# Kernel optimization log

Hardware: AMD Instinct MI355X
Metric: run time of the kernel (lower is better)

## Reference

```python
import jax, jax.numpy as jnp
import numpy as np

D_MODEL = 1024
N_HEADS = 16
D_HEAD = D_MODEL // N_HEADS
D_FF = 4096
B, T = 4, 2048
LN_EPS = 1e-5


def _layer_norm(x, gamma, beta):
    mu = jnp.mean(x, axis=-1, keepdims=True)
    var = jnp.var(x, axis=-1, keepdims=True)
    return (x - mu) * jax.lax.rsqrt(var + LN_EPS) * gamma + beta


def setup_inputs() -> dict:
    key = jax.random.key(0)
    ks = jax.random.split(key, 8)
    x = jax.random.normal(ks[0], (B, T, D_MODEL), dtype=jnp.float32)
    # causal mask: True = blocked (upper triangle above diagonal)
    attn_mask = ~jnp.tril(jnp.ones((T, T), dtype=bool))
    # xavier-uniform linear weights stored as [in, out] (pytorch applies x @ W.T)
    def xavier(k, fan_in, fan_out):
        lim = float(np.sqrt(6.0 / (fan_in + fan_out)))
        return jax.random.uniform(k, (fan_in, fan_out), jnp.float32, -lim, lim)
    Wq = xavier(ks[1], D_MODEL, D_MODEL); bq = jnp.zeros((D_MODEL,), jnp.float32)
    Wk = xavier(ks[2], D_MODEL, D_MODEL); bk = jnp.zeros((D_MODEL,), jnp.float32)
    Wv = xavier(ks[3], D_MODEL, D_MODEL); bv = jnp.zeros((D_MODEL,), jnp.float32)
    Wo = xavier(ks[4], D_MODEL, D_MODEL); bo = jnp.zeros((D_MODEL,), jnp.float32)
    W1 = xavier(ks[5], D_MODEL, D_FF); b1 = jnp.zeros((D_FF,), jnp.float32)
    W2 = 0.02 * jax.random.normal(ks[6], (D_FF, D_MODEL), jnp.float32)  # normal std=0.02 per _init_weights
    b2 = jnp.zeros((D_MODEL,), jnp.float32)
    g1 = jnp.ones((D_MODEL,), jnp.float32); be1 = jnp.zeros((D_MODEL,), jnp.float32)
    g2 = jnp.ones((D_MODEL,), jnp.float32); be2 = jnp.zeros((D_MODEL,), jnp.float32)
    return {"x": x, "attn_mask": attn_mask,
            "Wq": Wq, "bq": bq, "Wk": Wk, "bk": bk, "Wv": Wv, "bv": bv,
            "Wo": Wo, "bo": bo, "W1": W1, "b1": b1, "W2": W2, "b2": b2,
            "g1": g1, "be1": be1, "g2": g2, "be2": be2}


def reference(x, attn_mask, Wq, bq, Wk, bk, Wv, bv, Wo, bo, W1, b1, W2, b2, g1, be1, g2, be2):
    Bd, Td, Dd = x.shape
    residual = x
    x_n = _layer_norm(x, g1, be1)
    # projections -> (B, H, T, Dh)
    q = (x_n @ Wq + bq).reshape(Bd, Td, N_HEADS, D_HEAD).transpose(0, 2, 1, 3)
    k = (x_n @ Wk + bk).reshape(Bd, Td, N_HEADS, D_HEAD).transpose(0, 2, 1, 3)
    v = (x_n @ Wv + bv).reshape(Bd, Td, N_HEADS, D_HEAD).transpose(0, 2, 1, 3)
    scale = 1.0 / jnp.sqrt(jnp.asarray(D_HEAD, x.dtype))
    scores = jnp.einsum('bhqd,bhkd->bhqk', q, k) * scale  # (B,H,T,T)
    scores = jnp.where(attn_mask[None, None], -jnp.inf, scores)
    attn = jax.nn.softmax(scores, axis=-1)
    attn_out = jnp.einsum('bhqk,bhkd->bhqd', attn, v)
    attn_out = attn_out.transpose(0, 2, 1, 3).reshape(Bd, Td, Dd)
    attn_out = attn_out @ Wo + bo
    x = residual + attn_out  # dropout = identity (p=0 / eval)
    h = _layer_norm(x, g2, be2)
    h = jax.nn.gelu(h @ W1 + b1, approximate=False) @ W2 + b2
    return x + h
```

## Files before the change

kernel.cpp:

```cpp
#include <hip/hip_runtime.h>
#include <hip/hip_bf16.h>
#include <math.h>

#define TT   2048
#define DD   1024
#define HHD  16
#define FFD  4096
#define NTOK 8192

typedef __attribute__((ext_vector_type(8))) short bf16x8;
typedef __attribute__((ext_vector_type(4))) float f32x4;
typedef unsigned int u32;
#define AS(n) __attribute__((address_space(n)))

__device__ __forceinline__ unsigned short f2bf(float f) {
    u32 u = __builtin_bit_cast(u32, f);
    u += 0x7fffu + ((u >> 16) & 1u);
    return (unsigned short)(u >> 16);
}

__device__ __forceinline__ void gld_lds16(const void* g, void* l) {
    __builtin_amdgcn_global_load_lds((const AS(1) u32*)g, (AS(3) u32*)l, 16, 0, 0);
}

__device__ __forceinline__ int swz(int row) { return (row + (row >> 3)) & 7; }

__global__ __launch_bounds__(256) void wtrans(const float* __restrict__ W,
                                              unsigned short* __restrict__ Wt,
                                              int K, int N) {
    __shared__ float t[32][33];
    int tx = threadIdx.x & 31, ty = threadIdx.x >> 5;
    int n0 = blockIdx.x * 32, k0 = blockIdx.y * 32;
    #pragma unroll
    for (int i = 0; i < 32; i += 8)
        t[ty + i][tx] = W[(size_t)(k0 + ty + i) * N + n0 + tx];
    __syncthreads();
    #pragma unroll
    for (int i = 0; i < 32; i += 8)
        Wt[(size_t)(n0 + ty + i) * K + k0 + tx] = f2bf(t[tx][ty + i]);
}

__global__ __launch_bounds__(256) void ln_bf16(const float* __restrict__ x,
                                               const float* __restrict__ g,
                                               const float* __restrict__ be,
                                               unsigned short* __restrict__ y) {
    int tok = blockIdx.x, tid = threadIdx.x;
    float4 v = ((const float4*)(x + (size_t)tok * DD))[tid];
    float s  = v.x + v.y + v.z + v.w;
    float ss = v.x*v.x + v.y*v.y + v.z*v.z + v.w*v.w;
    #pragma unroll
    for (int m = 32; m >= 1; m >>= 1) { s += __shfl_xor(s, m); ss += __shfl_xor(ss, m); }
    __shared__ float red[8];
    if ((tid & 63) == 0) { red[tid >> 6] = s; red[4 + (tid >> 6)] = ss; }
    __syncthreads();
    s  = red[0] + red[1] + red[2] + red[3];
    ss = red[4] + red[5] + red[6] + red[7];
    float mu   = s * (1.0f / DD);
    float rstd = rsqrtf(ss * (1.0f / DD) - mu * mu + 1e-5f);
    float4 gv = ((const float4*)g)[tid];
    float4 bv = ((const float4*)be)[tid];
    ushort4 o;
    o.x = f2bf((v.x - mu) * rstd * gv.x + bv.x);
    o.y = f2bf((v.y - mu) * rstd * gv.y + bv.y);
    o.z = f2bf((v.z - mu) * rstd * gv.z + bv.z);
    o.w = f2bf((v.w - mu) * rstd * gv.w + bv.w);
    *(ushort4*)(y + (size_t)tok * DD + tid * 4) = o;
}

template <int MODE>
__global__ __launch_bounds__(256, 3) void gemm_bf16(const unsigned short* __restrict__ A,
                                                    const unsigned short* __restrict__ Bt,
                                                    const float* __restrict__ bias,
                                                    void* __restrict__ C,
                                                    const float* __restrict__ resid,
                                                    int M, int N, int K) {
    __shared__ __align__(16) unsigned short As[128 * 64];
    __shared__ __align__(16) unsigned short Bs[128 * 64];
    int tid = threadIdx.x, lane = tid & 63, w = tid >> 6;
    int wm = w >> 1, wn = w & 1;
    int m0 = blockIdx.y * 128, n0 = blockIdx.x * 128;
    int c = lane & 15, g = lane >> 4;

    f32x4 acc[4][4];
    f32x4 z4 = {0.f, 0.f, 0.f, 0.f};
    #pragma unroll
    for (int i = 0; i < 4; ++i)
        #pragma unroll
        for (int j = 0; j < 4; ++j) acc[i][j] = z4;

    const unsigned short* aSrc[4];
    const unsigned short* bSrc[4];
    int ldsOff[4];
    #pragma unroll
    for (int i = 0; i < 4; ++i) {
        int inst = w * 4 + i;
        int row  = inst * 8 + (lane >> 3);
        int kk   = ((lane & 7) ^ swz(row)) << 3;
        aSrc[i] = A  + (size_t)(m0 + row) * K + kk;
        bSrc[i] = Bt + (size_t)(n0 + row) * K + kk;
        ldsOff[i] = inst * 1024;
    }

    for (int k0 = 0; k0 < K; k0 += 64) {
        #pragma unroll
        for (int i = 0; i < 4; ++i) {
            gld_lds16(aSrc[i] + k0, (char*)As + ldsOff[i]);
            gld_lds16(bSrc[i] + k0, (char*)Bs + ldsOff[i]);
        }
        __syncthreads();
        #pragma unroll
        for (int ks = 0; ks < 2; ++ks) {
            bf16x8 af[4], bfr[4];
            int slot = ks * 4 + g;
            #pragma unroll
            for (int f = 0; f < 4; ++f) {
                int ra = wm * 64 + f * 16 + c;
                af[f]  = *(const bf16x8*)((const char*)As + ra * 128 + ((slot ^ swz(ra)) << 4));
                int rb = wn * 64 + f * 16 + c;
                bfr[f] = *(const bf16x8*)((const char*)Bs + rb * 128 + ((slot ^ swz(rb)) << 4));
            }
            #pragma unroll
            for (int i = 0; i < 4; ++i)
                #pragma unroll
                for (int j = 0; j < 4; ++j)
                    acc[i][j] = __builtin_amdgcn_mfma_f32_16x16x32_bf16(af[i], bfr[j], acc[i][j], 0, 0, 0);
        }
        __syncthreads();
    }

    float bcol[4];
    #pragma unroll
    for (int j = 0; j < 4; ++j) bcol[j] = bias[n0 + wn * 64 + j * 16 + c];
    #pragma unroll
    for (int i = 0; i < 4; ++i) {
        #pragma unroll
        for (int r = 0; r < 4; ++r) {
            int rowm = m0 + wm * 64 + i * 16 + g * 4 + r;
            #pragma unroll
            for (int j = 0; j < 4; ++j) {
                float val = acc[i][j][r] + bcol[j];
                int col = n0 + wn * 64 + j * 16 + c;
                if (MODE == 1) {
                    int b = rowm >> 11, t = rowm & 2047, h = col >> 6, d = col & 63;
                    ((unsigned short*)C)[(((size_t)((b << 4) + h) * TT + t) << 6) + d] = f2bf(val);
                } else if (MODE == 2) {
                    size_t idx = (size_t)rowm * N + col;
                    ((float*)C)[idx] = val + resid[idx];
                } else {
                    float ge = 0.5f * val * (1.0f + erff(val * 0.70710678118f));
                    ((unsigned short*)C)[(size_t)rowm * N + col] = f2bf(ge);
                }
            }
        }
    }
}

__global__ __launch_bounds__(256) void attn_bf16(const unsigned short* __restrict__ q,
                                                 const unsigned short* __restrict__ k,
                                                 const unsigned short* __restrict__ v,
                                                 unsigned short* __restrict__ ao) {
    __shared__ __align__(16) unsigned short Ks[64 * 64];
    __shared__ __align__(16) unsigned short Vt[64 * 64];
    __shared__ __align__(16) unsigned short Ps[4][16 * 64];
    int tid = threadIdx.x, lane = tid & 63, w = tid >> 6;
    int qt = blockIdx.x, bh = blockIdx.y;
    int q0 = qt * 64;
    size_t base = (size_t)bh * TT * 64;
    int c = lane & 15, g = lane >> 4;

    int qrow = q0 + w * 16 + c;
    bf16x8 qf[2];
    qf[0] = *(const bf16x8*)(q + base + (size_t)qrow * 64 + g * 8);
    qf[1] = *(const bf16x8*)(q + base + (size_t)qrow * 64 + 32 + g * 8);

    float m_i[4], l_i[4];
    f32x4 o[4];
    f32x4 z4 = {0.f, 0.f, 0.f, 0.f};
    #pragma unroll
    for (int j = 0; j < 4; ++j) { m_i[j] = -INFINITY; l_i[j] = 0.0f; o[j] = z4; }

    const unsigned short* kSrc[2];
    int kOff[2];
    #pragma unroll
    for (int i = 0; i < 2; ++i) {
        int inst = w * 2 + i;
        int row  = inst * 8 + (lane >> 3);
        kSrc[i] = k + base + (size_t)row * 64 + (((lane & 7) ^ swz(row)) << 3);
        kOff[i] = inst * 1024;
    }

    for (int kt = 0; kt <= qt; ++kt) {
        int kv0 = kt * 64;
        __syncthreads();
        #pragma unroll
        for (int i = 0; i < 2; ++i)
            gld_lds16(kSrc[i] + (size_t)kv0 * 64, (char*)Ks + kOff[i]);
        #pragma unroll
        for (int p = 0; p < 2; ++p) {
            int kvr = w * 16 + p * 8 + (lane >> 3);
            int d0  = (lane & 7) * 8;
            bf16x8 vv = *(const bf16x8*)(v + base + (size_t)(kv0 + kvr) * 64 + d0);
            #pragma unroll
            for (int e = 0; e < 8; ++e) {
                int dr = d0 + e;
                int byte = dr * 128 + ((((kvr >> 3) ^ swz(dr)) << 4)) + ((kvr & 7) << 1);
                *(unsigned short*)((char*)Vt + byte) = (unsigned short)vv[e];
            }
        }
        __syncthreads();

        f32x4 s[4];
        #pragma unroll
        for (int f = 0; f < 4; ++f) s[f] = z4;
        #pragma unroll
        for (int ks = 0; ks < 2; ++ks) {
            int slot = ks * 4 + g;
            #pragma unroll
            for (int f = 0; f < 4; ++f) {
                int rb = f * 16 + c;
                bf16x8 kf = *(const bf16x8*)((const char*)Ks + rb * 128 + ((slot ^ swz(rb)) << 4));
                s[f] = __builtin_amdgcn_mfma_f32_16x16x32_bf16(qf[ks], kf, s[f], 0, 0, 0);
            }
        }

        bool diag = (kt == qt);
        #pragma unroll
        for (int j = 0; j < 4; ++j) {
            int lq = g * 4 + j;
            int gq = q0 + w * 16 + lq;
            #pragma unroll
            for (int f = 0; f < 4; ++f) {
                float sv = s[f][j] * 0.125f;
                if (diag && (kv0 + f * 16 + c > gq)) sv = -INFINITY;
                s[f][j] = sv;
            }
            float mx = fmaxf(fmaxf(s[0][j], s[1][j]), fmaxf(s[2][j], s[3][j]));
            #pragma unroll
            for (int mm = 8; mm >= 1; mm >>= 1) mx = fmaxf(mx, __shfl_xor(mx, mm));
            float newm = fmaxf(m_i[j], mx);
            float al = __expf(m_i[j] - newm);
            float rs = 0.0f;
            #pragma unroll
            for (int f = 0; f < 4; ++f) {
                float p = __expf(s[f][j] - newm);
                s[f][j] = p;
                rs += p;
            }
            #pragma unroll
            for (int mm = 8; mm >= 1; mm >>= 1) rs += __shfl_xor(rs, mm);
            l_i[j] = l_i[j] * al + rs;
            m_i[j] = newm;
            #pragma unroll
            for (int f = 0; f < 4; ++f) {
                int col = f * 16 + c;
                int byte = lq * 128 + (((col >> 3) ^ swz(lq)) << 4) + ((col & 7) << 1);
                *(unsigned short*)((char*)Ps[w] + byte) = f2bf(s[f][j]);
            }
            #pragma unroll
            for (int fd = 0; fd < 4; ++fd) o[fd][j] *= al;
        }
        asm volatile("s_waitcnt lgkmcnt(0)" ::: "memory");
        __builtin_amdgcn_sched_barrier(0);

        #pragma unroll
        for (int ks = 0; ks < 2; ++ks) {
            int slot = ks * 4 + g;
            bf16x8 pa = *(const bf16x8*)((const char*)Ps[w] + c * 128 + ((slot ^ swz(c)) << 4));
            #pragma unroll
            for (int fd = 0; fd < 4; ++fd) {
                int rv = fd * 16 + c;
                bf16x8 vf = *(const bf16x8*)((const char*)Vt + rv * 128 + ((slot ^ swz(rv)) << 4));
                o[fd] = __builtin_amdgcn_mfma_f32_16x16x32_bf16(pa, vf, o[fd], 0, 0, 0);
            }
        }
    }

    int b = bh >> 4, h = bh & 15;
    #pragma unroll
    for (int fd = 0; fd < 4; ++fd)
        #pragma unroll
        for (int j = 0; j < 4; ++j) {
            int t = q0 + w * 16 + g * 4 + j;
            float val = o[fd][j] / l_i[j];
            ao[(((size_t)(b * TT + t)) << 10) + (h << 6) + fd * 16 + c] = f2bf(val);
        }
}

extern "C" void kernel_launch(void* const* d_in, const int* in_sizes, int n_in,
                              void* d_out, int out_size, void* d_ws, size_t ws_size,
                              hipStream_t stream) {
    const float* x   = (const float*)d_in[0];
    const float* Wq  = (const float*)d_in[2];
    const float* bq  = (const float*)d_in[3];
    const float* Wk  = (const float*)d_in[4];
    const float* bk  = (const float*)d_in[5];
    const float* Wv  = (const float*)d_in[6];
    const float* bv  = (const float*)d_in[7];
    const float* Wo  = (const float*)d_in[8];
    const float* bo  = (const float*)d_in[9];
    const float* W1  = (const float*)d_in[10];
    const float* b1  = (const float*)d_in[11];
    const float* W2  = (const float*)d_in[12];
    const float* b2  = (const float*)d_in[13];
    const float* g1  = (const float*)d_in[14];
    const float* be1 = (const float*)d_in[15];
    const float* g2  = (const float*)d_in[16];
    const float* be2 = (const float*)d_in[17];

    float* out = (float*)d_out;
    char* w = (char*)d_ws;
    const size_t MB = 1024 * 1024;
    unsigned short* xnb = (unsigned short*)(w);
    unsigned short* qb  = (unsigned short*)(w + 16 * MB);
    unsigned short* kb  = (unsigned short*)(w + 32 * MB);
    unsigned short* vb  = (unsigned short*)(w + 48 * MB);
    unsigned short* aob = (unsigned short*)(w + 64 * MB);
    unsigned short* wqt = (unsigned short*)(w + 80 * MB);
    unsigned short* wkt = wqt + 1 * MB;
    unsigned short* wvt = wqt + 2 * MB;
    unsigned short* wot = wqt + 3 * MB;
    unsigned short* w1t = wqt + 4 * MB;
    unsigned short* w2t = w1t + 4 * MB;
    unsigned short* h1  = qb;

    dim3 blk(256);
    wtrans<<<dim3(DD / 32, DD / 32), blk, 0, stream>>>(Wq, wqt, DD, DD);
    wtrans<<<dim3(DD / 32, DD / 32), blk, 0, stream>>>(Wk, wkt, DD, DD);
    wtrans<<<dim3(DD / 32, DD / 32), blk, 0, stream>>>(Wv, wvt, DD, DD);
    wtrans<<<dim3(DD / 32, DD / 32), blk, 0, stream>>>(Wo, wot, DD, DD);
    wtrans<<<dim3(FFD / 32, DD / 32), blk, 0, stream>>>(W1, w1t, DD, FFD);
    wtrans<<<dim3(DD / 32, FFD / 32), blk, 0, stream>>>(W2, w2t, FFD, DD);

    ln_bf16<<<NTOK, blk, 0, stream>>>(x, g1, be1, xnb);

    dim3 gD(DD / 128, NTOK / 128);
    dim3 gF(FFD / 128, NTOK / 128);
    gemm_bf16<1><<<gD, blk, 0, stream>>>(xnb, wqt, bq, qb, nullptr, NTOK, DD, DD);
    gemm_bf16<1><<<gD, blk, 0, stream>>>(xnb, wkt, bk, kb, nullptr, NTOK, DD, DD);
    gemm_bf16<1><<<gD, blk, 0, stream>>>(xnb, wvt, bv, vb, nullptr, NTOK, DD, DD);

    attn_bf16<<<dim3(TT / 64, 64), blk, 0, stream>>>(qb, kb, vb, aob);

    gemm_bf16<2><<<gD, blk, 0, stream>>>(aob, wot, bo, out, x, NTOK, DD, DD);
    ln_bf16<<<NTOK, blk, 0, stream>>>(out, g2, be2, xnb);
    gemm_bf16<3><<<gF, blk, 0, stream>>>(xnb, w1t, b1, h1, nullptr, NTOK, FFD, DD);
    gemm_bf16<2><<<gD, blk, 0, stream>>>(h1, w2t, b2, out, out, NTOK, DD, FFD);
}
```

Measured before the change: 705.9 us.

## Emit V pre-transposed from projection GEMM and double-buffer K/V in attention

The V projection now computes V^T by swapping GEMM operands, with a new epilogue mode that writes V as (b,h,d,t) and applies the bias per row. The attention kernel can then load V tiles straight into LDS with async global-to-LDS copies instead of a per-element transposed scatter. K/V tiles are double-buffered so the next tile's load overlaps the current compute. Each block handles a pair of causal query tiles (pr and 31-pr) to balance work, with a remapped bh order, MFMA priority hints and launch bounds for 4 blocks per CU. The cost is more LDS per block and a less cache-friendly transposed store pattern in the V GEMM epilogue.

```diff
diff --git a/kernel.cpp b/kernel.cpp
--- a/kernel.cpp
+++ b/kernel.cpp
@@ -129,16 +129,24 @@
     }
 
     float bcol[4];
-    #pragma unroll
-    for (int j = 0; j < 4; ++j) bcol[j] = bias[n0 + wn * 64 + j * 16 + c];
+    float4 brow[4];
+    if (MODE == 4) {
+        #pragma unroll
+        for (int i = 0; i < 4; ++i)
+            brow[i] = *(const float4*)&bias[m0 + wm * 64 + i * 16 + g * 4];
+    } else {
+        #pragma unroll
+        for (int j = 0; j < 4; ++j) bcol[j] = bias[n0 + wn * 64 + j * 16 + c];
+    }
     #pragma unroll
     for (int i = 0; i < 4; ++i) {
         #pragma unroll
         for (int r = 0; r < 4; ++r) {
             int rowm = m0 + wm * 64 + i * 16 + g * 4 + r;
+            float br = (MODE == 4) ? ((const float*)&brow[i])[r] : 0.0f;
             #pragma unroll
             for (int j = 0; j < 4; ++j) {
-                float val = acc[i][j][r] + bcol[j];
+                float val = acc[i][j][r] + ((MODE == 4) ? br : bcol[j]);
                 int col = n0 + wn * 64 + j * 16 + c;
                 if (MODE == 1) {
                     int b = rowm >> 11, t = rowm & 2047, h = col >> 6, d = col & 63;
@@ -146,144 +154,157 @@
                 } else if (MODE == 2) {
                     size_t idx = (size_t)rowm * N + col;
                     ((float*)C)[idx] = val + resid[idx];
-                } else {
+                } else if (MODE == 3) {
                     float ge = 0.5f * val * (1.0f + erff(val * 0.70710678118f));
                     ((unsigned short*)C)[(size_t)rowm * N + col] = f2bf(ge);
-                }
-            }
-        }
-    }
-}
-
-__global__ __launch_bounds__(256) void attn_bf16(const unsigned short* __restrict__ q,
-                                                 const unsigned short* __restrict__ k,
-                                                 const unsigned short* __restrict__ v,
-                                                 unsigned short* __restrict__ ao) {
-    __shared__ __align__(16) unsigned short Ks[64 * 64];
-    __shared__ __align__(16) unsigned short Vt[64 * 64];
+                } else {
+                    int b = col >> 11, t = col & 2047, h = rowm >> 6, d = rowm & 63;
+                    ((unsigned short*)C)[(((size_t)((b << 4) + h) * 64 + d) << 11) + t] = f2bf(val);
+                }
+            }
+        }
+    }
+}
+
+__global__ __launch_bounds__(256, 4) void attn_bf16(const unsigned short* __restrict__ q,
+                                                    const unsigned short* __restrict__ k,
+                                                    const unsigned short* __restrict__ vt,
+                                                    unsigned short* __restrict__ ao) {
+    __shared__ __align__(16) unsigned short Ks[2][64 * 64];
+    __shared__ __align__(16) unsigned short Vts[2][64 * 64];
     __shared__ __align__(16) unsigned short Ps[4][16 * 64];
     int tid = threadIdx.x, lane = tid & 63, w = tid >> 6;
-    int qt = blockIdx.x, bh = blockIdx.y;
-    int q0 = qt * 64;
-    size_t base = (size_t)bh * TT * 64;
+    int bid = blockIdx.x;
+    int bh  = (bid & 7) * 8 + ((bid >> 3) & 7);
+    int pr  = bid >> 6;
     int c = lane & 15, g = lane >> 4;
-
-    int qrow = q0 + w * 16 + c;
-    bf16x8 qf[2];
-    qf[0] = *(const bf16x8*)(q + base + (size_t)qrow * 64 + g * 8);
-    qf[1] = *(const bf16x8*)(q + base + (size_t)qrow * 64 + 32 + g * 8);
-
-    float m_i[4], l_i[4];
-    f32x4 o[4];
-    f32x4 z4 = {0.f, 0.f, 0.f, 0.f};
-    #pragma unroll
-    for (int j = 0; j < 4; ++j) { m_i[j] = -INFINITY; l_i[j] = 0.0f; o[j] = z4; }
+    size_t kbase = (size_t)bh * TT * 64;
+    size_t vbase = (size_t)bh * 64 * TT;
 
     const unsigned short* kSrc[2];
-    int kOff[2];
+    const unsigned short* vSrc[2];
+    int ldsOff[2];
     #pragma unroll
     for (int i = 0; i < 2; ++i) {
         int inst = w * 2 + i;
         int row  = inst * 8 + (lane >> 3);
-        kSrc[i] = k + base + (size_t)row * 64 + (((lane & 7) ^ swz(row)) << 3);
-        kOff[i] = inst * 1024;
-    }
-
-    for (int kt = 0; kt <= qt; ++kt) {
-        int kv0 = kt * 64;
+        int kk   = ((lane & 7) ^ swz(row)) << 3;
+        kSrc[i] = k  + kbase + (size_t)row * 64 + kk;
+        vSrc[i] = vt + vbase + (size_t)row * TT + kk;
+        ldsOff[i] = inst * 1024;
+    }
+
+    auto STAGE = [&](int buf, int kv0) {
+        #pragma unroll
+        for (int i = 0; i < 2; ++i) {
+            gld_lds16(kSrc[i] + (size_t)kv0 * 64, (char*)Ks[buf] + ldsOff[i]);
+            gld_lds16(vSrc[i] + kv0,              (char*)Vts[buf] + ldsOff[i]);
+        }
+    };
+
+    int b = bh >> 4, h = bh & 15;
+    f32x4 z4 = {0.f, 0.f, 0.f, 0.f};
+
+    for (int ph = 0; ph < 2; ++ph) {
+        int qt = ph ? (31 - pr) : pr;
+        int q0 = qt * 64;
+        int qrow = q0 + w * 16 + c;
+        bf16x8 qf[2];
+        qf[0] = *(const bf16x8*)(q + kbase + (size_t)qrow * 64 + g * 8);
+        qf[1] = *(const bf16x8*)(q + kbase + (size_t)qrow * 64 + 32 + g * 8);
+
+        float m_i[4], l_i[4];
+        f32x4 o[4];
+        #pragma unroll
+        for (int j = 0; j < 4; ++j) { m_i[j] = -INFINITY; l_i[j] = 0.0f; o[j] = z4; }
+
         __syncthreads();
-        #pragma unroll
-        for (int i = 0; i < 2; ++i)
-            gld_lds16(kSrc[i] + (size_t)kv0 * 64, (char*)Ks + kOff[i]);
-        #pragma unroll
-        for (int p = 0; p < 2; ++p) {
-            int kvr = w * 16 + p * 8 + (lane >> 3);
-            int d0  = (lane & 7) * 8;
-            bf16x8 vv = *(const bf16x8*)(v + base + (size_t)(kv0 + kvr) * 64 + d0);
-            #pragma unroll
-            for (int e = 0; e < 8; ++e) {
-                int dr = d0 + e;
-                int byte = dr * 128 + ((((kvr >> 3) ^ swz(dr)) << 4)) + ((kvr & 7) << 1);
-                *(unsigned short*)((char*)Vt + byte) = (unsigned short)vv[e];
-            }
-        }
-        __syncthreads();
-
-        f32x4 s[4];
-        #pragma unroll
-        for (int f = 0; f < 4; ++f) s[f] = z4;
-        #pragma unroll
-        for (int ks = 0; ks < 2; ++ks) {
-            int slot = ks * 4 + g;
-            #pragma unroll
-            for (int f = 0; f < 4; ++f) {
-                int rb = f * 16 + c;
-                bf16x8 kf = *(const bf16x8*)((const char*)Ks + rb * 128 + ((slot ^ swz(rb)) << 4));
-                s[f] = __builtin_amdgcn_mfma_f32_16x16x32_bf16(qf[ks], kf, s[f], 0, 0, 0);
-            }
-        }
-
-        bool diag = (kt == qt);
-        #pragma unroll
-        for (int j = 0; j < 4; ++j) {
-            int lq = g * 4 + j;
-            int gq = q0 + w * 16 + lq;
-            #pragma unroll
-            for (int f = 0; f < 4; ++f) {
-                float sv = s[f][j] * 0.125f;
-                if (diag && (kv0 + f * 16 + c > gq)) sv = -INFINITY;
-                s[f][j] = sv;
-            }
-            float mx = fmaxf(fmaxf(s[0][j], s[1][j]), fmaxf(s[2][j], s[3][j]));
-            #pragma unroll
-            for (int mm = 8; mm >= 1; mm >>= 1) mx = fmaxf(mx, __shfl_xor(mx, mm));
-            float newm = fmaxf(m_i[j], mx);
-            float al = __expf(m_i[j] - newm);
-            float rs = 0.0f;
-            #pragma unroll
-            for (int f = 0; f < 4; ++f) {
-                float p = __expf(s[f][j] - newm);
-                s[f][j] = p;
-                rs += p;
-            }
-            #pragma unroll
-            for (int mm = 8; mm >= 1; mm >>= 1) rs += __shfl_xor(rs, mm);
-            l_i[j] = l_i[j] * al + rs;
-            m_i[j] = newm;
-            #pragma unroll
-            for (int f = 0; f < 4; ++f) {
-                int col = f * 16 + c;
-                int byte = lq * 128 + (((col >> 3) ^ swz(lq)) << 4) + ((col & 7) << 1);
-                *(unsigned short*)((char*)Ps[w] + byte) = f2bf(s[f][j]);
-            }
-            #pragma unroll
-            for (int fd = 0; fd < 4; ++fd) o[fd][j] *= al;
-        }
-        asm volatile("s_waitcnt lgkmcnt(0)" ::: "memory");
-        __builtin_amdgcn_sched_barrier(0);
-
-        #pragma unroll
-        for (int ks = 0; ks < 2; ++ks) {
-            int slot = ks * 4 + g;
-            bf16x8 pa = *(const bf16x8*)((const char*)Ps[w] + c * 128 + ((slot ^ swz(c)) << 4));
-            #pragma unroll
-            for (int fd = 0; fd < 4; ++fd) {
-                int rv = fd * 16 + c;
-                bf16x8 vf = *(const bf16x8*)((const char*)Vt + rv * 128 + ((slot ^ swz(rv)) << 4));
-                o[fd] = __builtin_amdgcn_mfma_f32_16x16x32_bf16(pa, vf, o[fd], 0, 0, 0);
-            }
-        }
-    }
-
-    int b = bh >> 4, h = bh & 15;
-    #pragma unroll
-    for (int fd = 0; fd < 4; ++fd)
-        #pragma unroll
-        for (int j = 0; j < 4; ++j) {
-            int t = q0 + w * 16 + g * 4 + j;
-            float val = o[fd][j] / l_i[j];
-            ao[(((size_t)(b * TT + t)) << 10) + (h << 6) + fd * 16 + c] = f2bf(val);
-        }
+        STAGE(0, 0);
+
+        for (int kt = 0; kt <= qt; ++kt) {
+            int cur = kt & 1, kv0 = kt * 64;
+            __syncthreads();
+            if (kt < qt) STAGE(cur ^ 1, kv0 + 64);
+
+            f32x4 s[4];
+            #pragma unroll
+            for (int f = 0; f < 4; ++f) s[f] = z4;
+            __builtin_amdgcn_s_setprio(1);
+            #pragma unroll
+            for (int ks = 0; ks < 2; ++ks) {
+                int slot = ks * 4 + g;
+                #pragma unroll
+                for (int f = 0; f < 4; ++f) {
+                    int rb = f * 16 + c;
+                    bf16x8 kf = *(const bf16x8*)((const char*)Ks[cur] + rb * 128 + ((slot ^ swz(rb)) << 4));
+                    s[f] = __builtin_amdgcn_mfma_f32_16x16x32_bf16(qf[ks], kf, s[f], 0, 0, 0);
+                }
+            }
+            __builtin_amdgcn_s_setprio(0);
+
+            bool diag = (kt == qt);
+            #pragma unroll
+            for (int j = 0; j < 4; ++j) {
+                int lq = g * 4 + j;
+                int gq = q0 + w * 16 + lq;
+                #pragma unroll
+                for (int f = 0; f < 4; ++f) {
+                    float sv = s[f][j] * 0.125f;
+                    if (diag && (kv0 + f * 16 + c > gq)) sv = -INFINITY;
+                    s[f][j] = sv;
+                }
+                float mx = fmaxf(fmaxf(s[0][j], s[1][j]), fmaxf(s[2][j], s[3][j]));
+                #pragma unroll
+                for (int mm = 8; mm >= 1; mm >>= 1) mx = fmaxf(mx, __shfl_xor(mx, mm));
+                float newm = fmaxf(m_i[j], mx);
+                float al = __expf(m_i[j] - newm);
+                float rs = 0.0f;
+                #pragma unroll
+                for (int f = 0; f < 4; ++f) {
+                    float p = __expf(s[f][j] - newm);
+                    s[f][j] = p;
+                    rs += p;
+                }
+                #pragma unroll
+                for (int mm = 8; mm >= 1; mm >>= 1) rs += __shfl_xor(rs, mm);
+                l_i[j] = l_i[j] * al + rs;
+                m_i[j] = newm;
+                #pragma unroll
+                for (int f = 0; f < 4; ++f) {
+                    int col = f * 16 + c;
+                    int byte = lq * 128 + (((col >> 3) ^ swz(lq)) << 4) + ((col & 7) << 1);
+                    *(unsigned short*)((char*)Ps[w] + byte) = f2bf(s[f][j]);
+                }
+                #pragma unroll
+                for (int fd = 0; fd < 4; ++fd) o[fd][j] *= al;
+            }
+            asm volatile("s_waitcnt lgkmcnt(0)" ::: "memory");
+            __builtin_amdgcn_sched_barrier(0);
+
+            __builtin_amdgcn_s_setprio(1);
+            #pragma unroll
+            for (int ks = 0; ks < 2; ++ks) {
+                int slot = ks * 4 + g;
+                bf16x8 pa = *(const bf16x8*)((const char*)Ps[w] + c * 128 + ((slot ^ swz(c)) << 4));
+                #pragma unroll
+                for (int fd = 0; fd < 4; ++fd) {
+                    int rv = fd * 16 + c;
+                    bf16x8 vf = *(const bf16x8*)((const char*)Vts[cur] + rv * 128 + ((slot ^ swz(rv)) << 4));
+                    o[fd] = __builtin_amdgcn_mfma_f32_16x16x32_bf16(pa, vf, o[fd], 0, 0, 0);
+                }
+            }
+            __builtin_amdgcn_s_setprio(0);
+        }
+
+        #pragma unroll
+        for (int fd = 0; fd < 4; ++fd)
+            #pragma unroll
+            for (int j = 0; j < 4; ++j) {
+                int t = q0 + w * 16 + g * 4 + j;
+                float val = o[fd][j] / l_i[j];
+                ao[(((size_t)(b * TT + t)) << 10) + (h << 6) + fd * 16 + c] = f2bf(val);
+            }
+    }
 }
 
 extern "C" void kernel_launch(void* const* d_in, const int* in_sizes, int n_in,
@@ -335,11 +356,12 @@
 
     dim3 gD(DD / 128, NTOK / 128);
     dim3 gF(FFD / 128, NTOK / 128);
+    dim3 gV(NTOK / 128, DD / 128);
     gemm_bf16<1><<<gD, blk, 0, stream>>>(xnb, wqt, bq, qb, nullptr, NTOK, DD, DD);
     gemm_bf16<1><<<gD, blk, 0, stream>>>(xnb, wkt, bk, kb, nullptr, NTOK, DD, DD);
-    gemm_bf16<1><<<gD, blk, 0, stream>>>(xnb, wvt, bv, vb, nullptr, NTOK, DD, DD);
-
-    attn_bf16<<<dim3(TT / 64, 64), blk, 0, stream>>>(qb, kb, vb, aob);
+    gemm_bf16<4><<<gV, blk, 0, stream>>>(wvt, xnb, bv, vb, nullptr, DD, NTOK, DD);
+
+    attn_bf16<<<dim3(1024), blk, 0, stream>>>(qb, kb, vb, aob);
 
     gemm_bf16<2><<<gD, blk, 0, stream>>>(aob, wot, bo, out, x, NTOK, DD, DD);
     ln_bf16<<<NTOK, blk, 0, stream>>>(out, g2, be2, xnb);
```

Measured after the change: 586.4 us. 1.2x faster.
